# Optimization experiments

Measured on AMD Instinct MI355X. Metric: run time of the kernel, lower is better.

## Reference

```python
import jax, jax.numpy as jnp
import numpy as np

B, T, F, H, O = 8192, 10, 561, 256, 12


def _lstm_cell(x, h, c, Wih, Whh, bih, bhh):
    # PyTorch gate order: input, forget, cell(g), output
    gates = x @ Wih.T + bih + h @ Whh.T + bhh  # [B, 4H]
    i, f, g, o = jnp.split(gates, 4, axis=-1)
    c_new = jax.nn.sigmoid(f) * c + jax.nn.sigmoid(i) * jnp.tanh(g)
    h_new = jax.nn.sigmoid(o) * jnp.tanh(c_new)
    return h_new, c_new


def setup_inputs() -> dict:
    key = jax.random.key(0)
    ks = jax.random.split(key, 12)
    s_in = 1.0 / np.sqrt(F)
    s_h = 1.0 / np.sqrt(H)
    u = lambda k, shape, s: jax.random.uniform(k, shape, jnp.float32, -s, s)
    return {
        "inputs": jax.random.normal(ks[0], (B, T, F), jnp.float32),
        "W_inp": u(ks[1], (H, F), s_in), "b_inp": u(ks[2], (H,), s_in),
        "Wih0": u(ks[3], (4 * H, H), s_h), "Whh0": u(ks[4], (4 * H, H), s_h),
        "bih0": u(ks[5], (4 * H,), s_h), "bhh0": u(ks[6], (4 * H,), s_h),
        "Wih1": u(ks[7], (4 * H, H), s_h), "Whh1": u(ks[8], (4 * H, H), s_h),
        "bih1": u(ks[9], (4 * H,), s_h), "bhh1": u(ks[10], (4 * H,), s_h),
        "W_out": u(ks[11], (O, H), s_h), "b_out": jnp.zeros((O,), jnp.float32),
    }


def reference(inputs, W_inp, b_inp, Wih0, Whh0, bih0, bhh0,
              Wih1, Whh1, bih1, bhh1, W_out, b_out):
    b, t, _ = inputs.shape
    h = W_inp.shape[0]
    # input Linear applied to every timestep (same math as per-step self.inp)
    xp = jnp.einsum('btf,hf->bth', inputs, W_inp) + b_inp  # [B,T,H]

    def step(carry, x_t):
        h0, c0, h1, c1 = carry
        h0, c0 = _lstm_cell(x_t, h0, c0, Wih0, Whh0, bih0, bhh0)
        h1, c1 = _lstm_cell(h0, h1, c1, Wih1, Whh1, bih1, bhh1)
        return (h0, c0, h1, c1), h1

    z = jnp.zeros((b, h), inputs.dtype)
    (h0, c0, h1, c1), hs = jax.lax.scan(step, (z, z, z, z), jnp.swapaxes(xp, 0, 1))
    outputs = jnp.einsum('tbh,oh->bto', hs, W_out) + b_out  # [B,T,O]
    h_n = jnp.stack([h0, h1])  # [2,B,H] like torch LSTM hidden
    c_n = jnp.stack([c0, c1])
    return outputs, h_n, c_n
```

## Files before the change

kernel.cpp:

```cpp
#include <hip/hip_runtime.h>

#define BB 8192
#define TT 10
#define FF 561
#define FP 576
#define HH 256
#define OO 12

typedef __attribute__((ext_vector_type(8))) __bf16 bf16x8;
typedef __attribute__((ext_vector_type(4))) float f32x4;

__device__ __forceinline__ unsigned short f2bf(float f) {
  unsigned int u = __float_as_uint(f);
  u += 0x7fffu + ((u >> 16) & 1u);
  return (unsigned short)(u >> 16);
}
__device__ __forceinline__ float bf2f(unsigned short s) {
  return __uint_as_float(((unsigned int)s) << 16);
}
__device__ __forceinline__ float sigm(float x) { return 1.f / (1.f + __expf(-x)); }
__device__ __forceinline__ float tanh_fast(float x) { return 1.f - 2.f / (__expf(2.f * x) + 1.f); }

__device__ __forceinline__ void gl_lds16(const unsigned short* g, unsigned short* l) {
  __builtin_amdgcn_global_load_lds(
      (const __attribute__((address_space(1))) unsigned int*)g,
      (__attribute__((address_space(3))) unsigned int*)l, 16, 0, 0);
}

__global__ void conv_inputs(const float* __restrict__ in, unsigned short* __restrict__ Ain) {
  int idx = blockIdx.x * 256 + threadIdx.x;
  if (idx >= 81920 * 144) return;
  int c4 = (idx % 144) * 4;
  size_t row = idx / 144;
  const float* src = in + row * 561 + c4;
  ushort4 v;
  v.x = f2bf(c4 + 0 < 561 ? src[0] : 0.f);
  v.y = f2bf(c4 + 1 < 561 ? src[1] : 0.f);
  v.z = f2bf(c4 + 2 < 561 ? src[2] : 0.f);
  v.w = f2bf(c4 + 3 < 561 ? src[3] : 0.f);
  *(ushort4*)(Ain + row * 576 + c4) = v;
}

__global__ void conv_weights(const float* __restrict__ Winp,
                             const float* __restrict__ Wih0, const float* __restrict__ Whh0,
                             const float* __restrict__ Wih1, const float* __restrict__ Whh1,
                             const float* __restrict__ Wout,
                             unsigned short* __restrict__ Wib,
                             unsigned short* __restrict__ W0p,
                             unsigned short* __restrict__ W1p,
                             unsigned short* __restrict__ Wob) {
  int idx = blockIdx.x * 256 + threadIdx.x;
  if (idx < 256 * 576) {
    int kk = idx % 576, n = idx / 576;
    Wib[idx] = f2bf(kk < 561 ? Winp[n * 561 + kk] : 0.f);
    return;
  }
  idx -= 256 * 576;
  if (idx < 1024 * 512) {
    int kk = idx % 512, np = idx / 512;
    int h = (np >> 7) * 32 + (np & 31), g = (np >> 5) & 3;
    int sr = g * 256 + h;
    float v = kk < 256 ? Wih0[sr * 256 + kk] : Whh0[sr * 256 + kk - 256];
    W0p[idx] = f2bf(v);
    return;
  }
  idx -= 1024 * 512;
  if (idx < 1024 * 512) {
    int kk = idx % 512, np = idx / 512;
    int h = (np >> 7) * 32 + (np & 31), g = (np >> 5) & 3;
    int sr = g * 256 + h;
    float v = kk < 256 ? Wih1[sr * 256 + kk] : Whh1[sr * 256 + kk - 256];
    W1p[idx] = f2bf(v);
    return;
  }
  idx -= 1024 * 512;
  if (idx < 16 * 256) {
    int kk = idx % 256, o = idx / 256;
    Wob[idx] = f2bf(o < OO ? Wout[o * 256 + kk] : 0.f);
  }
}

template <int MODE>
__global__ __launch_bounds__(256, 2) void gemm_k(
    const unsigned short* __restrict__ A0, int lda0, int K0,
    const unsigned short* __restrict__ A1, int lda1,
    const unsigned short* __restrict__ W, int K,
    const float* __restrict__ biasA, const float* __restrict__ biasB,
    float* __restrict__ cbuf,
    unsigned short* __restrict__ hout,
    float* __restrict__ hf32, float* __restrict__ cf32) {
  __shared__ __align__(16) unsigned short As[128 * 32];
  __shared__ __align__(16) unsigned short Bs[128 * 32];
  const int tid = threadIdx.x;
  const int w = tid >> 6, lane = tid & 63, quad = lane >> 4, l15 = lane & 15;
  const int mb = blockIdx.x, nb = blockIdx.y;

  f32x4 acc[2][8];
#pragma unroll
  for (int i = 0; i < 2; ++i)
#pragma unroll
    for (int j = 0; j < 8; ++j) acc[i][j] = (f32x4){0.f, 0.f, 0.f, 0.f};

  const int r0 = tid >> 2;
  const int cc = (tid & 3) * 8;

  for (int k0 = 0; k0 < K; k0 += 32) {
    __syncthreads();
    const unsigned short* Asrc;
    int ldA, kk;
    if (k0 < K0) { Asrc = A0; ldA = lda0; kk = k0; }
    else         { Asrc = A1; ldA = lda1; kk = k0 - K0; }
    gl_lds16(Asrc + (size_t)(mb * 128 + r0) * ldA + kk + cc, &As[tid * 8]);
    gl_lds16(Asrc + (size_t)(mb * 128 + 64 + r0) * ldA + kk + cc, &As[2048 + tid * 8]);
    gl_lds16(W + (size_t)(nb * 128 + r0) * K + k0 + cc, &Bs[tid * 8]);
    gl_lds16(W + (size_t)(nb * 128 + 64 + r0) * K + k0 + cc, &Bs[2048 + tid * 8]);
    __syncthreads();

    bf16x8 af[2], bfr[8];
#pragma unroll
    for (int mt = 0; mt < 2; ++mt)
      af[mt] = *(const bf16x8*)&As[(w * 32 + mt * 16 + l15) * 32 + quad * 8];
#pragma unroll
    for (int nt = 0; nt < 8; ++nt)
      bfr[nt] = *(const bf16x8*)&Bs[(nt * 16 + l15) * 32 + quad * 8];
#pragma unroll
    for (int mt = 0; mt < 2; ++mt)
#pragma unroll
      for (int nt = 0; nt < 8; ++nt)
        acc[mt][nt] = __builtin_amdgcn_mfma_f32_16x16x32_bf16(af[mt], bfr[nt], acc[mt][nt], 0, 0, 0);
  }

  if constexpr (MODE == 0) {
#pragma unroll
    for (int mt = 0; mt < 2; ++mt) {
      int rowb = mb * 128 + w * 32 + mt * 16 + quad * 4;
#pragma unroll
      for (int nt = 0; nt < 8; ++nt) {
        int col = nb * 128 + nt * 16 + l15;
        float bv = biasA[col];
#pragma unroll
        for (int r = 0; r < 4; ++r)
          hout[(size_t)(rowb + r) * HH + col] = f2bf(acc[mt][nt][r] + bv);
      }
    }
  } else {
#pragma unroll
    for (int hb = 0; hb < 2; ++hb) {
      int hg = nb * 32 + hb * 16 + l15;
      float bI = biasA[hg] + biasB[hg];
      float bF = biasA[256 + hg] + biasB[256 + hg];
      float bG = biasA[512 + hg] + biasB[512 + hg];
      float bO = biasA[768 + hg] + biasB[768 + hg];
#pragma unroll
      for (int mt = 0; mt < 2; ++mt) {
        int rowb = mb * 128 + w * 32 + mt * 16 + quad * 4;
#pragma unroll
        for (int r = 0; r < 4; ++r) {
          size_t idx = (size_t)(rowb + r) * HH + hg;
          float xi = acc[mt][0 + hb][r] + bI;
          float xf = acc[mt][2 + hb][r] + bF;
          float xg = acc[mt][4 + hb][r] + bG;
          float xo = acc[mt][6 + hb][r] + bO;
          float c_old = cbuf[idx];
          float cn = sigm(xf) * c_old + sigm(xi) * tanh_fast(xg);
          float hn = sigm(xo) * tanh_fast(cn);
          cbuf[idx] = cn;
          hout[idx] = f2bf(hn);
          if (hf32) hf32[idx] = hn;
          if (cf32) cf32[idx] = cn;
        }
      }
    }
  }
}

__global__ __launch_bounds__(256) void out_gemm_mfma(
    const unsigned short* __restrict__ hs,
    const unsigned short* __restrict__ Wob,
    const float* __restrict__ bout,
    float* __restrict__ out) {
  const int tid = threadIdx.x;
  const int w = tid >> 6, lane = tid & 63, quad = lane >> 4, l15 = lane & 15;
  const int m0 = blockIdx.x * 64 + w * 16;
  const unsigned short* arow = hs + (size_t)(m0 + l15 + BB) * HH + quad * 8;
  const unsigned short* brow = Wob + l15 * HH + quad * 8;
  f32x4 acc = (f32x4){0.f, 0.f, 0.f, 0.f};
#pragma unroll
  for (int k0 = 0; k0 < 8; ++k0) {
    bf16x8 a = *(const bf16x8*)(arow + k0 * 32);
    bf16x8 b = *(const bf16x8*)(brow + k0 * 32);
    acc = __builtin_amdgcn_mfma_f32_16x16x32_bf16(a, b, acc, 0, 0, 0);
  }
  const int o = l15;
  if (o < OO) {
    float bv = bout[o];
#pragma unroll
    for (int r = 0; r < 4; ++r) {
      int m = m0 + quad * 4 + r;
      int b = m & (BB - 1);
      int t = m >> 13;
      out[((size_t)b * TT + t) * OO + o] = acc[r] + bv;
    }
  }
}

extern "C" void kernel_launch(void* const* d_in, const int* in_sizes, int n_in,
                              void* d_out, int out_size, void* d_ws, size_t ws_size,
                              hipStream_t stream) {
  const float* inputs = (const float*)d_in[0];
  const float* W_inp  = (const float*)d_in[1];
  const float* b_inp  = (const float*)d_in[2];
  const float* Wih0   = (const float*)d_in[3];
  const float* Whh0   = (const float*)d_in[4];
  const float* bih0   = (const float*)d_in[5];
  const float* bhh0   = (const float*)d_in[6];
  const float* Wih1   = (const float*)d_in[7];
  const float* Whh1   = (const float*)d_in[8];
  const float* bih1   = (const float*)d_in[9];
  const float* bhh1   = (const float*)d_in[10];
  const float* W_out  = (const float*)d_in[11];
  const float* b_out  = (const float*)d_in[12];
  float* out = (float*)d_out;

  char* ws = (char*)d_ws;
  size_t off = 0;
  auto alloc = [&](size_t bytes) {
    char* p = ws + off;
    off += (bytes + 255) & ~(size_t)255;
    return p;
  };
  unsigned short* Ain = (unsigned short*)alloc((size_t)81920 * FP * 2);
  unsigned short* xp  = (unsigned short*)alloc((size_t)81920 * HH * 2);
  unsigned short* Wib = (unsigned short*)alloc((size_t)256 * FP * 2);
  unsigned short* W0p = (unsigned short*)alloc((size_t)1024 * 512 * 2);
  unsigned short* W1p = (unsigned short*)alloc((size_t)1024 * 512 * 2);
  unsigned short* Wob = (unsigned short*)alloc((size_t)16 * HH * 2);
  unsigned short* h0s = (unsigned short*)alloc((size_t)2 * BB * HH * 2);
  unsigned short* hs  = (unsigned short*)alloc((size_t)(TT + 1) * BB * HH * 2);
  float* c0 = (float*)alloc((size_t)BB * HH * 4);
  float* c1 = (float*)alloc((size_t)BB * HH * 4);

  hipMemsetAsync(h0s, 0, (size_t)BB * HH * 2, stream);
  hipMemsetAsync(hs, 0, (size_t)BB * HH * 2, stream);
  hipMemsetAsync(c0, 0, (size_t)BB * HH * 4, stream);
  hipMemsetAsync(c1, 0, (size_t)BB * HH * 4, stream);

  conv_inputs<<<(81920 * 144 + 255) / 256, 256, 0, stream>>>(inputs, Ain);
  {
    int nthr = 256 * 576 + 2 * 1024 * 512 + 16 * 256;
    conv_weights<<<(nthr + 255) / 256, 256, 0, stream>>>(W_inp, Wih0, Whh0, Wih1, Whh1,
                                                         W_out, Wib, W0p, W1p, Wob);
  }

  gemm_k<0><<<dim3(640, 2), 256, 0, stream>>>(
      Ain, FP, FP, (const unsigned short*)nullptr, 0,
      Wib, FP, b_inp, (const float*)nullptr,
      (float*)nullptr, xp, (float*)nullptr, (float*)nullptr);

  float* hn_out = out + (size_t)BB * TT * OO;
  float* cn_out = hn_out + (size_t)2 * BB * HH;

  for (int t = 0; t < TT; ++t) {
    const unsigned short* h0_prev = h0s + (size_t)(t & 1) * BB * HH;
    unsigned short* h0_new       = h0s + (size_t)((t + 1) & 1) * BB * HH;
    const unsigned short* xpt = xp + (size_t)t * HH;
    const unsigned short* h1_prev = hs + (size_t)t * BB * HH;
    unsigned short* h1_new        = hs + (size_t)(t + 1) * BB * HH;
    bool last = (t == TT - 1);

    gemm_k<1><<<dim3(64, 8), 256, 0, stream>>>(
        xpt, TT * HH, 256, h0_prev, HH,
        W0p, 512, bih0, bhh0, c0, h0_new,
        last ? hn_out : (float*)nullptr,
        last ? cn_out : (float*)nullptr);

    gemm_k<1><<<dim3(64, 8), 256, 0, stream>>>(
        h0_new, HH, 256, h1_prev, HH,
        W1p, 512, bih1, bhh1, c1, h1_new,
        last ? hn_out + (size_t)BB * HH : (float*)nullptr,
        last ? cn_out + (size_t)BB * HH : (float*)nullptr);
  }

  out_gemm_mfma<<<1280, 256, 0, stream>>>(hs, Wob, b_out, out);
}
```

Measured before the change: 781.2 us.

## Wavefront-fuse LSTM layers per launch with double-buffered LDS and XCD block mapping

Each recurrent launch now runs layer-0 step s and layer-1 step s-1 back to back in the same blocks. This cuts the number of recurrent launches from twenty to eleven, and the next job's first tile is prefetched while the current epilogue runs. The GEMM main loops are double-buffered in LDS so the global-to-LDS copy overlaps the MFMAs. Block indices are remapped so neighbouring tiles land on the same XCD. In exchange, LDS use per block doubles, and each block does twice the serial work per launch.

Result: no change. 780.5 us (-0.1%).

```diff
diff --git a/kernel.cpp b/kernel.cpp
--- a/kernel.cpp
+++ b/kernel.cpp
@@ -15,9 +15,6 @@
   u += 0x7fffu + ((u >> 16) & 1u);
   return (unsigned short)(u >> 16);
 }
-__device__ __forceinline__ float bf2f(unsigned short s) {
-  return __uint_as_float(((unsigned int)s) << 16);
-}
 __device__ __forceinline__ float sigm(float x) { return 1.f / (1.f + __expf(-x)); }
 __device__ __forceinline__ float tanh_fast(float x) { return 1.f - 2.f / (__expf(2.f * x) + 1.f); }
 
@@ -25,6 +22,22 @@
   __builtin_amdgcn_global_load_lds(
       (const __attribute__((address_space(1))) unsigned int*)g,
       (__attribute__((address_space(3))) unsigned int*)l, 16, 0, 0);
+}
+
+__device__ __forceinline__ void mfma_tile(const unsigned short* as, const unsigned short* bs,
+                                          int w, int quad, int l15, f32x4 (&acc)[2][8]) {
+  bf16x8 af[2], bfr[8];
+#pragma unroll
+  for (int mt = 0; mt < 2; ++mt)
+    af[mt] = *(const bf16x8*)&as[(w * 32 + mt * 16 + l15) * 32 + quad * 8];
+#pragma unroll
+  for (int nt = 0; nt < 8; ++nt)
+    bfr[nt] = *(const bf16x8*)&bs[(nt * 16 + l15) * 32 + quad * 8];
+#pragma unroll
+  for (int mt = 0; mt < 2; ++mt)
+#pragma unroll
+    for (int nt = 0; nt < 8; ++nt)
+      acc[mt][nt] = __builtin_amdgcn_mfma_f32_16x16x32_bf16(af[mt], bfr[nt], acc[mt][nt], 0, 0, 0);
 }
 
 __global__ void conv_inputs(const float* __restrict__ in, unsigned short* __restrict__ Ain) {
@@ -80,20 +93,24 @@
   }
 }
 
-template <int MODE>
-__global__ __launch_bounds__(256, 2) void gemm_k(
-    const unsigned short* __restrict__ A0, int lda0, int K0,
-    const unsigned short* __restrict__ A1, int lda1,
-    const unsigned short* __restrict__ W, int K,
-    const float* __restrict__ biasA, const float* __restrict__ biasB,
-    float* __restrict__ cbuf,
-    unsigned short* __restrict__ hout,
-    float* __restrict__ hf32, float* __restrict__ cf32) {
-  __shared__ __align__(16) unsigned short As[128 * 32];
-  __shared__ __align__(16) unsigned short Bs[128 * 32];
+__global__ __launch_bounds__(256, 2) void gemm_xp(
+    const unsigned short* __restrict__ A, const unsigned short* __restrict__ W,
+    const float* __restrict__ bias, unsigned short* __restrict__ xp) {
+  __shared__ __align__(16) unsigned short As[2][128 * 32];
+  __shared__ __align__(16) unsigned short Bs[2][128 * 32];
   const int tid = threadIdx.x;
   const int w = tid >> 6, lane = tid & 63, quad = lane >> 4, l15 = lane & 15;
-  const int mb = blockIdx.x, nb = blockIdx.y;
+  const int flat = blockIdx.x;
+  const int xcd = flat & 7, kb = flat >> 3;
+  const int nb = kb & 1, mb = xcd * 80 + (kb >> 1);
+  const int r0 = tid >> 2, cc = (tid & 3) * 8;
+
+  auto stage = [&](int buf, int k0) {
+    gl_lds16(A + (size_t)(mb * 128 + r0) * FP + k0 + cc, &As[buf][tid * 8]);
+    gl_lds16(A + (size_t)(mb * 128 + 64 + r0) * FP + k0 + cc, &As[buf][2048 + tid * 8]);
+    gl_lds16(W + (size_t)(nb * 128 + r0) * FP + k0 + cc, &Bs[buf][tid * 8]);
+    gl_lds16(W + (size_t)(nb * 128 + 64 + r0) * FP + k0 + cc, &Bs[buf][2048 + tid * 8]);
+  };
 
   f32x4 acc[2][8];
 #pragma unroll
@@ -101,73 +118,108 @@
 #pragma unroll
     for (int j = 0; j < 8; ++j) acc[i][j] = (f32x4){0.f, 0.f, 0.f, 0.f};
 
-  const int r0 = tid >> 2;
-  const int cc = (tid & 3) * 8;
-
-  for (int k0 = 0; k0 < K; k0 += 32) {
+  stage(0, 0);
+  __syncthreads();
+  int cur = 0;
+#pragma unroll
+  for (int ks = 0; ks < 17; ++ks) {
+    stage(cur ^ 1, (ks + 1) * 32);
+    mfma_tile(&As[cur][0], &Bs[cur][0], w, quad, l15, acc);
     __syncthreads();
-    const unsigned short* Asrc;
-    int ldA, kk;
-    if (k0 < K0) { Asrc = A0; ldA = lda0; kk = k0; }
-    else         { Asrc = A1; ldA = lda1; kk = k0 - K0; }
-    gl_lds16(Asrc + (size_t)(mb * 128 + r0) * ldA + kk + cc, &As[tid * 8]);
-    gl_lds16(Asrc + (size_t)(mb * 128 + 64 + r0) * ldA + kk + cc, &As[2048 + tid * 8]);
-    gl_lds16(W + (size_t)(nb * 128 + r0) * K + k0 + cc, &Bs[tid * 8]);
-    gl_lds16(W + (size_t)(nb * 128 + 64 + r0) * K + k0 + cc, &Bs[2048 + tid * 8]);
+    cur ^= 1;
+  }
+  mfma_tile(&As[cur][0], &Bs[cur][0], w, quad, l15, acc);
+
+#pragma unroll
+  for (int mt = 0; mt < 2; ++mt) {
+    int rowb = mb * 128 + w * 32 + mt * 16 + quad * 4;
+#pragma unroll
+    for (int nt = 0; nt < 8; ++nt) {
+      int col = nb * 128 + nt * 16 + l15;
+      float bv = bias[col];
+#pragma unroll
+      for (int r = 0; r < 4; ++r)
+        xp[(size_t)(rowb + r) * HH + col] = f2bf(acc[mt][nt][r] + bv);
+    }
+  }
+}
+
+struct LstmJob {
+  const unsigned short* A0; int lda0;
+  const unsigned short* A1;
+  const unsigned short* W;
+  const float* bA; const float* bB;
+  float* cbuf;
+  unsigned short* hout;
+  float* hf32; float* cf32;
+};
+
+__global__ __launch_bounds__(256, 2) void lstm_step(LstmJob j0, LstmJob j1, int njobs) {
+  __shared__ __align__(16) unsigned short As[2][128 * 32];
+  __shared__ __align__(16) unsigned short Bs[2][128 * 32];
+  const int tid = threadIdx.x;
+  const int w = tid >> 6, lane = tid & 63, quad = lane >> 4, l15 = lane & 15;
+  const int flat = blockIdx.x;
+  const int xcd = flat & 7, kb = flat >> 3;
+  const int nb = kb >> 3, mb = xcd * 8 + (kb & 7);
+  const int r0 = tid >> 2, cc = (tid & 3) * 8;
+
+  auto stage = [&](const LstmJob& J, int buf, int k0) {
+    const unsigned short* Asrc; int ldA, kk;
+    if (k0 < 256) { Asrc = J.A0; ldA = J.lda0; kk = k0; }
+    else          { Asrc = J.A1; ldA = HH;     kk = k0 - 256; }
+    gl_lds16(Asrc + (size_t)(mb * 128 + r0) * ldA + kk + cc, &As[buf][tid * 8]);
+    gl_lds16(Asrc + (size_t)(mb * 128 + 64 + r0) * ldA + kk + cc, &As[buf][2048 + tid * 8]);
+    gl_lds16(J.W + (size_t)(nb * 128 + r0) * 512 + k0 + cc, &Bs[buf][tid * 8]);
+    gl_lds16(J.W + (size_t)(nb * 128 + 64 + r0) * 512 + k0 + cc, &Bs[buf][2048 + tid * 8]);
+  };
+
+  stage(j0, 0, 0);
+
+  for (int job = 0; job < njobs; ++job) {
+    const LstmJob J = job ? j1 : j0;
+    f32x4 acc[2][8];
+#pragma unroll
+    for (int i = 0; i < 2; ++i)
+#pragma unroll
+      for (int j = 0; j < 8; ++j) acc[i][j] = (f32x4){0.f, 0.f, 0.f, 0.f};
+
     __syncthreads();
-
-    bf16x8 af[2], bfr[8];
-#pragma unroll
-    for (int mt = 0; mt < 2; ++mt)
-      af[mt] = *(const bf16x8*)&As[(w * 32 + mt * 16 + l15) * 32 + quad * 8];
-#pragma unroll
-    for (int nt = 0; nt < 8; ++nt)
-      bfr[nt] = *(const bf16x8*)&Bs[(nt * 16 + l15) * 32 + quad * 8];
-#pragma unroll
-    for (int mt = 0; mt < 2; ++mt)
-#pragma unroll
-      for (int nt = 0; nt < 8; ++nt)
-        acc[mt][nt] = __builtin_amdgcn_mfma_f32_16x16x32_bf16(af[mt], bfr[nt], acc[mt][nt], 0, 0, 0);
-  }
-
-  if constexpr (MODE == 0) {
-#pragma unroll
-    for (int mt = 0; mt < 2; ++mt) {
-      int rowb = mb * 128 + w * 32 + mt * 16 + quad * 4;
-#pragma unroll
-      for (int nt = 0; nt < 8; ++nt) {
-        int col = nb * 128 + nt * 16 + l15;
-        float bv = biasA[col];
-#pragma unroll
-        for (int r = 0; r < 4; ++r)
-          hout[(size_t)(rowb + r) * HH + col] = f2bf(acc[mt][nt][r] + bv);
-      }
-    }
-  } else {
+    int cur = 0;
+#pragma unroll
+    for (int ks = 0; ks < 15; ++ks) {
+      stage(J, cur ^ 1, (ks + 1) * 32);
+      mfma_tile(&As[cur][0], &Bs[cur][0], w, quad, l15, acc);
+      __syncthreads();
+      cur ^= 1;
+    }
+    mfma_tile(&As[cur][0], &Bs[cur][0], w, quad, l15, acc);
+
+    if (job + 1 < njobs) stage(j1, 0, 0);
+
 #pragma unroll
     for (int hb = 0; hb < 2; ++hb) {
-      int hg = nb * 32 + hb * 16 + l15;
-      float bI = biasA[hg] + biasB[hg];
-      float bF = biasA[256 + hg] + biasB[256 + hg];
-      float bG = biasA[512 + hg] + biasB[512 + hg];
-      float bO = biasA[768 + hg] + biasB[768 + hg];
+      const int hg = nb * 32 + hb * 16 + l15;
+      const float bI = J.bA[hg] + J.bB[hg];
+      const float bF = J.bA[256 + hg] + J.bB[256 + hg];
+      const float bG = J.bA[512 + hg] + J.bB[512 + hg];
+      const float bO = J.bA[768 + hg] + J.bB[768 + hg];
 #pragma unroll
       for (int mt = 0; mt < 2; ++mt) {
-        int rowb = mb * 128 + w * 32 + mt * 16 + quad * 4;
+        const int rowb = mb * 128 + w * 32 + mt * 16 + quad * 4;
 #pragma unroll
         for (int r = 0; r < 4; ++r) {
-          size_t idx = (size_t)(rowb + r) * HH + hg;
-          float xi = acc[mt][0 + hb][r] + bI;
-          float xf = acc[mt][2 + hb][r] + bF;
-          float xg = acc[mt][4 + hb][r] + bG;
-          float xo = acc[mt][6 + hb][r] + bO;
-          float c_old = cbuf[idx];
-          float cn = sigm(xf) * c_old + sigm(xi) * tanh_fast(xg);
-          float hn = sigm(xo) * tanh_fast(cn);
-          cbuf[idx] = cn;
-          hout[idx] = f2bf(hn);
-          if (hf32) hf32[idx] = hn;
-          if (cf32) cf32[idx] = cn;
+          const size_t idx = (size_t)(rowb + r) * HH + hg;
+          const float xi = acc[mt][0 + hb][r] + bI;
+          const float xf = acc[mt][2 + hb][r] + bF;
+          const float xg = acc[mt][4 + hb][r] + bG;
+          const float xo = acc[mt][6 + hb][r] + bO;
+          const float c_old = J.cbuf[idx];
+          const float cn = sigm(xf) * c_old + sigm(xi) * tanh_fast(xg);
+          const float hn = sigm(xo) * tanh_fast(cn);
+          J.cbuf[idx] = cn;
+          J.hout[idx] = f2bf(hn);
+          if (J.hf32) { J.hf32[idx] = hn; J.cf32[idx] = cn; }
         }
       }
     }
@@ -252,33 +304,35 @@
                                                          W_out, Wib, W0p, W1p, Wob);
   }
 
-  gemm_k<0><<<dim3(640, 2), 256, 0, stream>>>(
-      Ain, FP, FP, (const unsigned short*)nullptr, 0,
-      Wib, FP, b_inp, (const float*)nullptr,
-      (float*)nullptr, xp, (float*)nullptr, (float*)nullptr);
+  gemm_xp<<<1280, 256, 0, stream>>>(Ain, Wib, b_inp, xp);
 
   float* hn_out = out + (size_t)BB * TT * OO;
   float* cn_out = hn_out + (size_t)2 * BB * HH;
 
-  for (int t = 0; t < TT; ++t) {
-    const unsigned short* h0_prev = h0s + (size_t)(t & 1) * BB * HH;
-    unsigned short* h0_new       = h0s + (size_t)((t + 1) & 1) * BB * HH;
-    const unsigned short* xpt = xp + (size_t)t * HH;
-    const unsigned short* h1_prev = hs + (size_t)t * BB * HH;
-    unsigned short* h1_new        = hs + (size_t)(t + 1) * BB * HH;
-    bool last = (t == TT - 1);
-
-    gemm_k<1><<<dim3(64, 8), 256, 0, stream>>>(
-        xpt, TT * HH, 256, h0_prev, HH,
-        W0p, 512, bih0, bhh0, c0, h0_new,
-        last ? hn_out : (float*)nullptr,
-        last ? cn_out : (float*)nullptr);
-
-    gemm_k<1><<<dim3(64, 8), 256, 0, stream>>>(
-        h0_new, HH, 256, h1_prev, HH,
-        W1p, 512, bih1, bhh1, c1, h1_new,
-        last ? hn_out + (size_t)BB * HH : (float*)nullptr,
-        last ? cn_out + (size_t)BB * HH : (float*)nullptr);
+  for (int s = 0; s <= TT; ++s) {
+    LstmJob jobs[2];
+    int nj = 0;
+    if (s < TT) {
+      int t = s;
+      jobs[nj++] = LstmJob{
+          xp + (size_t)t * HH, TT * HH,
+          h0s + (size_t)(t & 1) * BB * HH,
+          W0p, bih0, bhh0, c0,
+          h0s + (size_t)((t + 1) & 1) * BB * HH,
+          (t == TT - 1) ? hn_out : nullptr,
+          (t == TT - 1) ? cn_out : nullptr};
+    }
+    if (s > 0) {
+      int t = s - 1;
+      jobs[nj++] = LstmJob{
+          h0s + (size_t)((t + 1) & 1) * BB * HH, HH,
+          hs + (size_t)t * BB * HH,
+          W1p, bih1, bhh1, c1,
+          hs + (size_t)(t + 1) * BB * HH,
+          (t == TT - 1) ? hn_out + (size_t)BB * HH : nullptr,
+          (t == TT - 1) ? cn_out + (size_t)BB * HH : nullptr};
+    }
+    lstm_step<<<512, 256, 0, stream>>>(jobs[0], nj == 2 ? jobs[1] : jobs[0], nj);
   }
 
   out_gemm_mfma<<<1280, 256, 0, stream>>>(hs, Wob, b_out, out);
```
